# Performance work log

Measured on AMD Instinct MI355X. Metric: run time of the kernel, lower is better.

## Reference

```python
import jax, jax.numpy as jnp
import numpy as np

B, C, L = 8, 256, 2048
RED = 8
CQK = C // RED  # 32


def setup_inputs() -> dict:
    key = jax.random.key(0)
    ks = jax.random.split(key, 8)
    s = 0.05
    x = jax.random.normal(ks[0], (B, C, L), dtype=jnp.float32)
    Wq = jax.random.normal(ks[1], (CQK, C), dtype=jnp.float32) * s
    bq = jax.random.normal(ks[2], (CQK,), dtype=jnp.float32) * s
    Wk = jax.random.normal(ks[3], (CQK, C), dtype=jnp.float32) * s
    bk = jax.random.normal(ks[4], (CQK,), dtype=jnp.float32) * s
    Wv = jax.random.normal(ks[5], (C, C), dtype=jnp.float32) * s
    bv = jax.random.normal(ks[6], (C,), dtype=jnp.float32) * s
    gamma = jnp.asarray([0.5], dtype=jnp.float32)  # learned scalar (init 0 in torch)
    return {"x": x, "Wq": Wq, "bq": bq, "Wk": Wk, "bk": bk, "Wv": Wv, "bv": bv, "gamma": gamma}


def reference(x, Wq, bq, Wk, bk, Wv, bv, gamma):
    # 1x1 Conv1d == channel-mixing matmul: [O,C] x [B,C,L] -> [B,O,L]
    q = jnp.einsum('oc,bcl->bol', Wq, x) + bq[:, None]   # [B,CQK,L]
    k = jnp.einsum('oc,bcl->bol', Wk, x) + bk[:, None]   # [B,CQK,L]
    v = jnp.einsum('oc,bcl->bol', Wv, x) + bv[:, None]   # [B,C,L]
    # attn[b,i,j] = softmax_j( q(:,i) . k(:,j) )  -- NOTE: no 1/sqrt(d) scaling
    scores = jnp.einsum('bci,bcj->bij', q, k)            # [B,L,L]
    attn = jax.nn.softmax(scores, axis=-1)
    # out[b,c,i] = sum_j v[b,c,j] * attn[b,i,j]
    out = jnp.einsum('bcj,bij->bci', v, attn)            # [B,C,L]
    return gamma[0] * out + x
```

## Files before the change

### kernel.cpp

```cpp
#include <hip/hip_runtime.h>

#define B 8
#define C 256
#define L 2048
#define CQK 32
#define SSEG 4
#define JSEG (L / SSEG)
#define NT (JSEG / 32)
#define SM_SHIFT2 28.8539008f

typedef unsigned short u16;
typedef __attribute__((ext_vector_type(8))) short bf8;
typedef __attribute__((ext_vector_type(4))) float f4;

__device__ __forceinline__ u16 f2bf(float f) {
    union { float f; unsigned u; } v; v.f = f;
    unsigned r = v.u + 0x7FFFu + ((v.u >> 16) & 1u);
    return (u16)(r >> 16);
}
__device__ __forceinline__ float bfl(unsigned u) {
    union { unsigned u; float f; } v; v.u = u << 16; return v.f;
}
__device__ __forceinline__ float bfh(unsigned u) {
    union { unsigned u; float f; } v; v.u = u & 0xFFFF0000u; return v.f;
}
__device__ __forceinline__ unsigned cvtpk(float lo, float hi) {
    unsigned r;
    asm("v_cvt_pk_bf16_f32 %0, %1, %2" : "=v"(r) : "v"(lo), "v"(hi));
    return r;
}
__device__ __forceinline__ float ex2(float x) {
    float r;
    asm("v_exp_f32 %0, %1" : "=v"(r) : "v"(x));
    return r;
}

__device__ __forceinline__ void gld16(const u16* gp, u16* lp) {
    auto* g1 = (const __attribute__((address_space(1))) u16*)gp;
    auto* l3 = (__attribute__((address_space(3))) u16*)lp;
    __builtin_amdgcn_global_load_lds(g1, l3, 16, 0, 0);
}
__device__ __forceinline__ void wait_vm0() {
    asm volatile("s_waitcnt vmcnt(0)" ::: "memory");
    __builtin_amdgcn_sched_barrier(0);
}
__device__ __forceinline__ void wait_lgkm0() {
    asm volatile("s_waitcnt lgkmcnt(0)" ::: "memory");
    __builtin_amdgcn_sched_barrier(0);
}
__device__ __forceinline__ void bar() {
    __builtin_amdgcn_sched_barrier(0);
    __builtin_amdgcn_s_barrier();
    __builtin_amdgcn_sched_barrier(0);
}

__global__ __launch_bounds__(256) void wconv(
    const float* __restrict__ Wq, const float* __restrict__ bq,
    const float* __restrict__ Wk, const float* __restrict__ bk,
    const float* __restrict__ Wv, const float* __restrict__ bv,
    u16* __restrict__ Wall, float* __restrict__ ball)
{
    const int idx = (blockIdx.x * 256 + threadIdx.x) * 4;
    const int row = idx >> 8, c = idx & 255;
    const float* s;
    if (row < 32)      s = Wq + row * C + c;
    else if (row < 64) s = Wk + (row - 32) * C + c;
    else               s = Wv + (row - 64) * C + c;
    const float4 v = *(const float4*)s;
    uint2 o;
    o.x = f2bf(v.x) | ((unsigned)f2bf(v.y) << 16);
    o.y = f2bf(v.z) | ((unsigned)f2bf(v.w) << 16);
    *(uint2*)(Wall + idx) = o;
    if (blockIdx.x == 0) {
        for (int i = threadIdx.x; i < 320; i += 256)
            ball[i] = (i < 32) ? bq[i] : (i < 64) ? bk[i - 32] : bv[i - 64];
    }
}

__global__ __launch_bounds__(256) void xconv(const float* __restrict__ x,
                                             u16* __restrict__ xt)
{
    __shared__ float tile[64][65];
    const int b = blockIdx.z, c0 = blockIdx.y * 64, l0 = blockIdx.x * 64;
    const int t = threadIdx.x;
    const int ln = t & 63, w = t >> 6;
#pragma unroll
    for (int i = 0; i < 16; i++) {
        const int c = w * 16 + i;
        tile[c][ln] = x[((size_t)(b * C + c0 + c)) * L + l0 + ln];
    }
    __syncthreads();
    const int lrow = t >> 2, q = t & 3;
    unsigned o[8];
#pragma unroll
    for (int jj = 0; jj < 8; jj++) {
        const float a0 = tile[q * 16 + jj * 2][lrow];
        const float a1 = tile[q * 16 + jj * 2 + 1][lrow];
        o[jj] = f2bf(a0) | ((unsigned)f2bf(a1) << 16);
    }
    u16* dst = xt + ((size_t)(b * L + l0 + lrow)) * 256 + c0 + q * 16;
    *(uint4*)(dst)     = make_uint4(o[0], o[1], o[2], o[3]);
    *(uint4*)(dst + 8) = make_uint4(o[4], o[5], o[6], o[7]);
}

__global__ __launch_bounds__(256) void proj(
    const u16* __restrict__ xt, const u16* __restrict__ Wall,
    const float* __restrict__ ball, u16* __restrict__ qt,
    u16* __restrict__ kt, u16* __restrict__ vv)
{
    __shared__ u16 xlds[32 * 256];
    const int b = blockIdx.y, l0 = blockIdx.x * 32;
    const int t = threadIdx.x, w = t >> 6, ln = t & 63;
    const int lc = ln & 15, g = ln >> 4;

#pragma unroll
    for (int mm = 0; mm < 4; mm++) {
        const int cg = t + mm * 256;
        const int lrow = cg >> 5, phys = cg & 31;
        const int logical = (phys & 24) | ((phys & 7) ^ (lrow & 7));
        gld16(xt + ((size_t)(b * L + l0 + lrow)) * 256 + logical * 8,
              xlds + (size_t)(w * 64 + mm * 256) * 8);
    }
    __syncthreads();

    f4 acc[5][2];
#pragma unroll
    for (int rt = 0; rt < 5; rt++) {
        const int row0 = (w * 5 + rt) * 16 + g * 4;
        const float4 bi = *(const float4*)(ball + row0);
#pragma unroll
        for (int ct = 0; ct < 2; ct++) {
            acc[rt][ct].x = bi.x; acc[rt][ct].y = bi.y;
            acc[rt][ct].z = bi.z; acc[rt][ct].w = bi.w;
        }
    }

#pragma unroll
    for (int k = 0; k < 8; k++) {
        bf8 bfr[2];
#pragma unroll
        for (int ct = 0; ct < 2; ct++) {
            const int lrow = ct * 16 + lc;
            const int lchunk = k * 4 + g;
            const int phys = (lchunk & 24) | ((lchunk & 7) ^ (lrow & 7));
            bfr[ct] = *(const bf8*)(xlds + (size_t)lrow * 256 + phys * 8);
        }
#pragma unroll
        for (int rt = 0; rt < 5; rt++) {
            const bf8 af = *(const bf8*)(Wall +
                (size_t)((w * 5 + rt) * 16 + lc) * 256 + k * 32 + g * 8);
#pragma unroll
            for (int ct = 0; ct < 2; ct++)
                acc[rt][ct] = __builtin_amdgcn_mfma_f32_16x16x32_bf16(
                    af, bfr[ct], acc[rt][ct], 0, 0, 0);
        }
    }

    const float Q_SCALE = 1.44269504f;
#pragma unroll
    for (int rt = 0; rt < 5; rt++) {
        const int rg = w * 5 + rt;
        const int row0 = rg * 16 + g * 4;
#pragma unroll
        for (int ct = 0; ct < 2; ct++) {
            const int l = l0 + ct * 16 + lc;
            const f4 a = acc[rt][ct];
            if (rg < 2) {
                uint2 o;
                o.x = f2bf(a.x * Q_SCALE) | ((unsigned)f2bf(a.y * Q_SCALE) << 16);
                o.y = f2bf(a.z * Q_SCALE) | ((unsigned)f2bf(a.w * Q_SCALE) << 16);
                *(uint2*)(qt + ((size_t)(b * L + l)) * 32 + row0) = o;
            } else if (rg < 4) {
                uint2 o;
                o.x = f2bf(a.x) | ((unsigned)f2bf(a.y) << 16);
                o.y = f2bf(a.z) | ((unsigned)f2bf(a.w) << 16);
                *(uint2*)(kt + ((size_t)(b * L + l)) * 32 + (row0 - 32)) = o;
            } else {
                const int c = row0 - 64;
                vv[((size_t)(b * C + c + 0)) * L + l] = f2bf(a.x);
                vv[((size_t)(b * C + c + 1)) * L + l] = f2bf(a.y);
                vv[((size_t)(b * C + c + 2)) * L + l] = f2bf(a.z);
                vv[((size_t)(b * C + c + 3)) * L + l] = f2bf(a.w);
            }
        }
    }
}

__global__ __launch_bounds__(512, 4) void attn(
    const u16* __restrict__ qt, const u16* __restrict__ kt,
    const u16* __restrict__ vv, u16* __restrict__ po,
    float* __restrict__ plsum)
{
    __shared__ u16 vsw[8][2][1024];
    __shared__ u16 ps[64][40];
    __shared__ float fl[64];

    const int fid = blockIdx.x;
    const int win = fid & 31, bx = fid >> 5;
    const int b = win >> 2, sidx = win & 3;
    const int t = threadIdx.x, w = t >> 6, ln = t & 63;
    const int lc = ln & 15, g = ln >> 4;
    const int i0 = bx * 64;
    const int js = sidx * JSEG;
    const int wc0 = w * 32;
    const int tb = (b * 32 + bx) * SSEG + sidx;

    const int r0 = ln >> 2, s0 = ln & 3;
    const int gch = s0 ^ (r0 & 3) ^ ((r0 >> 2) & 3);
    const u16* vsrc = vv + ((size_t)(b * C + wc0 + r0)) * L + js + gch * 8;

    f4 acc[4][2];
    const f4 fz = {0.f, 0.f, 0.f, 0.f};
#pragma unroll
    for (int it = 0; it < 4; it++)
#pragma unroll
        for (int ct = 0; ct < 2; ct++) acc[it][ct] = fz;
    float lsum = 0.f;

    bf8 qf = {}, kf0 = {}, kf1 = {}, kn0 = {}, kn1 = {};
    const u16* kb = kt;
    if (w < 4) {
        qf = *(const bf8*)(qt + ((size_t)(b * L + i0 + w * 16 + lc)) * 32 + g * 8);
        kb = kt + ((size_t)(b * L + js + lc)) * 32 + g * 8;
        kn0 = *(const bf8*)(kb);
        kn1 = *(const bf8*)(kb + 16 * 32);
    }

    auto stage = [&](int buf, int jt) {
        const u16* s = vsrc + jt * 32;
        u16* d = &vsw[w][buf][0];
        gld16(s, d);
        gld16(s + (size_t)16 * L, d + 512);
    };

    stage(0, 0);
    int cur = 0;

    const int sread = (g ^ (lc & 3) ^ ((lc >> 2) & 3)) * 8;

#pragma unroll 1
    for (int jt = 0; jt < NT; jt++) {
        wait_vm0();
        bar();
        if (jt + 1 < NT) stage(cur ^ 1, jt + 1);

        if (w < 4) {
            kf0 = kn0; kf1 = kn1;
            if (jt + 1 < NT) {
                kn0 = *(const bf8*)(kb + (size_t)((jt + 1) * 32) * 32);
                kn1 = *(const bf8*)(kb + (size_t)((jt + 1) * 32 + 16) * 32);
            }
            const f4 sA = __builtin_amdgcn_mfma_f32_16x16x32_bf16(kf0, qf, fz, 0, 0, 0);
            const f4 sB = __builtin_amdgcn_mfma_f32_16x16x32_bf16(kf1, qf, fz, 0, 0, 0);
            const float p0 = ex2(sA.x - SM_SHIFT2);
            const float p1 = ex2(sA.y - SM_SHIFT2);
            const float p2 = ex2(sA.z - SM_SHIFT2);
            const float p3 = ex2(sA.w - SM_SHIFT2);
            const float p4 = ex2(sB.x - SM_SHIFT2);
            const float p5 = ex2(sB.y - SM_SHIFT2);
            const float p6 = ex2(sB.z - SM_SHIFT2);
            const float p7 = ex2(sB.w - SM_SHIFT2);
            uint2 oa, ob;
            oa.x = cvtpk(p0, p1); oa.y = cvtpk(p2, p3);
            ob.x = cvtpk(p4, p5); ob.y = cvtpk(p6, p7);
            *(uint2*)(&ps[w * 16 + lc][g * 4]) = oa;
            *(uint2*)(&ps[w * 16 + lc][16 + g * 4]) = ob;
            float psum = ((p0 + p1) + (p2 + p3)) + ((p4 + p5) + (p6 + p7));
            psum += __shfl_xor(psum, 16);
            psum += __shfl_xor(psum, 32);
            lsum += psum;
        }

        wait_lgkm0();
        bar();

        const u16* rb = &vsw[w][cur][0];
        __builtin_amdgcn_s_setprio(1);
#pragma unroll
        for (int ct = 0; ct < 2; ct++) {
            const bf8 vfr = *(const bf8*)(rb + ct * 512 + lc * 32 + sread);
#pragma unroll
            for (int it = 0; it < 4; it++) {
                const bf8 paf = *(const bf8*)(&ps[it * 16 + lc][0] + g * 8);
                acc[it][ct] = __builtin_amdgcn_mfma_f32_16x16x32_bf16(
                    paf, vfr, acc[it][ct], 0, 0, 0);
            }
        }
        __builtin_amdgcn_s_setprio(0);
        cur ^= 1;
    }

    if (w < 4) {
        fl[w * 16 + lc] = 1.0f / lsum;
        if (g == 0) plsum[(size_t)tb * 64 + w * 16 + lc] = lsum;
    }
    __syncthreads();
    u16* pob = po + (size_t)tb * 16384 + (size_t)(w & 1) * 2048
                  + ((size_t)(w >> 1) * 64 + g * 16 + lc) * 8;
#pragma unroll
    for (int it = 0; it < 4; it++) {
        const float4 iv = *(const float4*)&fl[it * 16 + g * 4];
        const f4 a0 = acc[it][0];
        const f4 a1 = acc[it][1];
        uint4 o;
        o.x = cvtpk(a0.x * iv.x, a0.y * iv.y);
        o.y = cvtpk(a0.z * iv.z, a0.w * iv.w);
        o.z = cvtpk(a1.x * iv.x, a1.y * iv.y);
        o.w = cvtpk(a1.z * iv.z, a1.w * iv.w);
        *(uint4*)(pob + (size_t)it * 4096) = o;
    }
}

__global__ __launch_bounds__(256) void combine(
    const u16* __restrict__ po, const float* __restrict__ plsum,
    const float* __restrict__ x, const float* __restrict__ gamma_p,
    float* __restrict__ out)
{
    __shared__ float raw[4][16];
    __shared__ float wts[4][16];
    const int bx = blockIdx.x, b = blockIdx.y, z = blockIdx.z;
    const int t = threadIdx.x, wq = t >> 6, ln = t & 63;
    const int lc = ln & 15, g = ln >> 4;
    const int tbase = (b * 32 + bx) * SSEG;

    if (t < 64)
        raw[t >> 4][t & 15] = plsum[(size_t)(tbase + (t >> 4)) * 64 + z * 16 + (t & 15)];
    __syncthreads();
    if (t < 16) {
        const float l0 = raw[0][t], l1 = raw[1][t], l2 = raw[2][t], l3 = raw[3][t];
        const float inv = 1.0f / (((l0 + l1) + (l2 + l3)));
        wts[0][t] = l0 * inv; wts[1][t] = l1 * inv;
        wts[2][t] = l2 * inv; wts[3][t] = l3 * inv;
    }
    __syncthreads();

    f4 tot[4];
    const f4 fz = {0.f, 0.f, 0.f, 0.f};
#pragma unroll
    for (int ct = 0; ct < 4; ct++) tot[ct] = fz;

#pragma unroll
    for (int s = 0; s < SSEG; s++) {
        const u16* base = po + ((size_t)(tbase + s) * 2048 + (size_t)z * 2 * 256 + t) * 8;
        const uint4 q0 = *(const uint4*)base;
        const uint4 q1 = *(const uint4*)(base + 2048);
        const float4 wv = *(const float4*)&wts[s][g * 4];
        tot[0].x += wv.x * bfl(q0.x); tot[0].y += wv.y * bfh(q0.x);
        tot[0].z += wv.z * bfl(q0.y); tot[0].w += wv.w * bfh(q0.y);
        tot[1].x += wv.x * bfl(q0.z); tot[1].y += wv.y * bfh(q0.z);
        tot[1].z += wv.z * bfl(q0.w); tot[1].w += wv.w * bfh(q0.w);
        tot[2].x += wv.x * bfl(q1.x); tot[2].y += wv.y * bfh(q1.x);
        tot[2].z += wv.z * bfl(q1.y); tot[2].w += wv.w * bfh(q1.y);
        tot[3].x += wv.x * bfl(q1.z); tot[3].y += wv.y * bfh(q1.z);
        tot[3].z += wv.z * bfl(q1.w); tot[3].w += wv.w * bfh(q1.w);
    }

    const float gmm = gamma_p[0];
#pragma unroll
    for (int ct = 0; ct < 4; ct++) {
        const int c = wq * 64 + ct * 16 + lc;
        const size_t adr = ((size_t)(b * C + c)) * L + bx * 64 + z * 16 + g * 4;
        const float4 xv = *(const float4*)(x + adr);
        float4 o;
        o.x = gmm * tot[ct].x + xv.x;
        o.y = gmm * tot[ct].y + xv.y;
        o.z = gmm * tot[ct].z + xv.z;
        o.w = gmm * tot[ct].w + xv.w;
        *(float4*)(out + adr) = o;
    }
}

extern "C" void kernel_launch(void* const* d_in, const int* in_sizes, int n_in,
                              void* d_out, int out_size, void* d_ws, size_t ws_size,
                              hipStream_t stream) {
    const float* x  = (const float*)d_in[0];
    const float* Wq = (const float*)d_in[1];
    const float* bq = (const float*)d_in[2];
    const float* Wk = (const float*)d_in[3];
    const float* bk = (const float*)d_in[4];
    const float* Wv = (const float*)d_in[5];
    const float* bv = (const float*)d_in[6];
    const float* gm = (const float*)d_in[7];
    float* out = (float*)d_out;

    u16* vvp  = (u16*)d_ws;
    u16* qtp  = vvp + (size_t)B * C * L;
    u16* ktp  = qtp + (size_t)B * L * CQK;
    u16* Wall = ktp + (size_t)B * L * CQK;
    float* ball = (float*)(Wall + 320 * 256);
    u16* xt   = Wall + 320 * 256 + 640;
    u16* po   = xt;
    float* plsum = (float*)(po + (size_t)B * 32 * SSEG * 2048 * 8);

    wconv<<<80, 256, 0, stream>>>(Wq, bq, Wk, bk, Wv, bv, Wall, ball);
    xconv<<<dim3(L / 64, C / 64, B), 256, 0, stream>>>(x, xt);
    proj<<<dim3(L / 32, B), 256, 0, stream>>>(xt, Wall, ball, qtp, ktp, vvp);
    attn<<<1024, 512, 0, stream>>>(qtp, ktp, vvp, po, plsum);
    combine<<<dim3(L / 64, B, SSEG), 256, 0, stream>>>(po, plsum, x, gm, out);
}
```

Before: 77.73 us.

## Double-buffer P tile and drop per-iteration barrier with deeper load pipelining

The P tile in shared memory is now double-buffered by iteration parity, so the barrier at the top of each loop iteration can be removed. The next V tile's async load to LDS is issued before waiting, and a partial `vmcnt(2)` wait keeps it in flight. K fragments are now loaded with inline-asm global loads issued right after the score MFMAs, replacing the register prefetch copies. The intent is to cut synchronisation stalls and hide global-load latency. In exchange it uses more LDS and depends on exact hand-counted vmcnt ordering.

```diff
diff --git a/kernel.cpp b/kernel.cpp
--- a/kernel.cpp
+++ b/kernel.cpp
@@ -42,6 +42,10 @@
 }
 __device__ __forceinline__ void wait_vm0() {
     asm volatile("s_waitcnt vmcnt(0)" ::: "memory");
+    __builtin_amdgcn_sched_barrier(0);
+}
+__device__ __forceinline__ void wait_vm2() {
+    asm volatile("s_waitcnt vmcnt(2)" ::: "memory");
     __builtin_amdgcn_sched_barrier(0);
 }
 __device__ __forceinline__ void wait_lgkm0() {
@@ -192,7 +196,7 @@
     float* __restrict__ plsum)
 {
     __shared__ u16 vsw[8][2][1024];
-    __shared__ u16 ps[64][40];
+    __shared__ u16 ps[2][64][40];
     __shared__ float fl[64];
 
     const int fid = blockIdx.x;
@@ -217,13 +221,11 @@
         for (int ct = 0; ct < 2; ct++) acc[it][ct] = fz;
     float lsum = 0.f;
 
-    bf8 qf = {}, kf0 = {}, kf1 = {}, kn0 = {}, kn1 = {};
+    bf8 qf = {}, kf0 = {}, kf1 = {};
     const u16* kb = kt;
     if (w < 4) {
         qf = *(const bf8*)(qt + ((size_t)(b * L + i0 + w * 16 + lc)) * 32 + g * 8);
         kb = kt + ((size_t)(b * L + js + lc)) * 32 + g * 8;
-        kn0 = *(const bf8*)(kb);
-        kn1 = *(const bf8*)(kb + 16 * 32);
     }
 
     auto stage = [&](int buf, int jt) {
@@ -232,26 +234,32 @@
         gld16(s, d);
         gld16(s + (size_t)16 * L, d + 512);
     };
+    auto kload = [&](int jt) {
+        asm volatile("global_load_dwordx4 %0, %1, off"
+                     : "=&v"(kf0) : "v"(kb + (size_t)(jt * 32) * 32) : "memory");
+        asm volatile("global_load_dwordx4 %0, %1, off"
+                     : "=&v"(kf1) : "v"(kb + (size_t)(jt * 32 + 16) * 32) : "memory");
+    };
 
     stage(0, 0);
+    if (w < 4) kload(0);
     int cur = 0;
 
     const int sread = (g ^ (lc & 3) ^ ((lc >> 2) & 3)) * 8;
 
 #pragma unroll 1
     for (int jt = 0; jt < NT; jt++) {
-        wait_vm0();
-        bar();
-        if (jt + 1 < NT) stage(cur ^ 1, jt + 1);
+        if (jt + 1 < NT) {
+            stage(cur ^ 1, jt + 1);
+            wait_vm2();
+        } else {
+            wait_vm0();
+        }
 
         if (w < 4) {
-            kf0 = kn0; kf1 = kn1;
-            if (jt + 1 < NT) {
-                kn0 = *(const bf8*)(kb + (size_t)((jt + 1) * 32) * 32);
-                kn1 = *(const bf8*)(kb + (size_t)((jt + 1) * 32 + 16) * 32);
-            }
             const f4 sA = __builtin_amdgcn_mfma_f32_16x16x32_bf16(kf0, qf, fz, 0, 0, 0);
             const f4 sB = __builtin_amdgcn_mfma_f32_16x16x32_bf16(kf1, qf, fz, 0, 0, 0);
+            if (jt + 1 < NT) kload(jt + 1);
             const float p0 = ex2(sA.x - SM_SHIFT2);
             const float p1 = ex2(sA.y - SM_SHIFT2);
             const float p2 = ex2(sA.z - SM_SHIFT2);
@@ -263,8 +271,8 @@
             uint2 oa, ob;
             oa.x = cvtpk(p0, p1); oa.y = cvtpk(p2, p3);
             ob.x = cvtpk(p4, p5); ob.y = cvtpk(p6, p7);
-            *(uint2*)(&ps[w * 16 + lc][g * 4]) = oa;
-            *(uint2*)(&ps[w * 16 + lc][16 + g * 4]) = ob;
+            *(uint2*)(&ps[jt & 1][w * 16 + lc][g * 4]) = oa;
+            *(uint2*)(&ps[jt & 1][w * 16 + lc][16 + g * 4]) = ob;
             float psum = ((p0 + p1) + (p2 + p3)) + ((p4 + p5) + (p6 + p7));
             psum += __shfl_xor(psum, 16);
             psum += __shfl_xor(psum, 32);
@@ -281,7 +289,7 @@
             const bf8 vfr = *(const bf8*)(rb + ct * 512 + lc * 32 + sread);
 #pragma unroll
             for (int it = 0; it < 4; it++) {
-                const bf8 paf = *(const bf8*)(&ps[it * 16 + lc][0] + g * 8);
+                const bf8 paf = *(const bf8*)(&ps[jt & 1][it * 16 + lc][0] + g * 8);
                 acc[it][ct] = __builtin_amdgcn_mfma_f32_16x16x32_bf16(
                     paf, vfr, acc[it][ct], 0, 0, 0);
             }
```

Result: faster. 73.64 us (-5.3%).
